# Performance work log

Hardware: AMD Instinct MI355X
Metric: run time of the kernel (lower is better)

## Reference

```python
import jax, jax.numpy as jnp
import numpy as np

B, LQ, LD, H, C = 128, 32, 512, 768, 128


def setup_inputs() -> dict:
    key = jax.random.key(0)
    ks = jax.random.split(key, 8)
    return {
        "query_hidden": jax.random.normal(ks[0], (B, LQ, H), dtype=jnp.float32),
        "doc_hidden": jax.random.normal(ks[1], (B, LD, H), dtype=jnp.float32),
        "query_mask": jax.random.randint(ks[2], (B, LQ), 0, 2, dtype=jnp.int32),
        "doc_mask": jax.random.randint(ks[3], (B, LD), 0, 2, dtype=jnp.int32),
        "W_comp": jax.random.normal(ks[4], (H, C), dtype=jnp.float32) * (1.0 / np.sqrt(H)),
        "b_comp": jax.random.normal(ks[5], (C,), dtype=jnp.float32) * 0.02,
        "w_stop": jax.random.normal(ks[6], (C, 1), dtype=jnp.float32) * (1.0 / np.sqrt(C)),
        "b_stop": jnp.ones((1,), dtype=jnp.float32),  # nn.init.constant_(bias, 1)
        "score_merger": jnp.zeros((1,), dtype=jnp.float32),
    }


def reference(query_hidden, doc_hidden, query_mask, doc_mask,
              W_comp, b_comp, w_stop, b_stop, score_merger):
    qm = query_mask.astype(bool)  # [B, LQ]
    dm = doc_mask.astype(bool)    # [B, LD]

    # encode_shared: CLS vec is the UNcompressed hidden state at position 0
    q_cls = query_hidden[:, 0, :]  # [B, H]
    d_cls = doc_hidden[:, 0, :]    # [B, H]

    # compressor (Linear H->C)
    q_vecs = jnp.einsum('blh,hc->blc', query_hidden, W_comp) + b_comp  # [B, LQ, C]
    d_tok = jnp.einsum('blh,hc->blc', doc_hidden, W_comp) + b_comp     # [B, LD, C]

    # encode_query: zero masked query tokens
    q_vecs = q_vecs * qm[..., None]

    # encode_doc: stopword reducer (relu of Linear C->1), then importance + mask
    importance = jax.nn.relu(jnp.einsum('blc,co->blo', d_tok, w_stop) + b_stop)  # [B, LD, 1]
    d_vecs = d_tok * importance * dm[..., None]

    # CLS score: dot product of (uncompressed) CLS vectors
    cls_score = jnp.sum(q_cls * d_cls, axis=-1)  # [B]

    # term score: MaxSim over doc tokens, masked sum over query tokens
    scores = jnp.einsum('bqc,bkc->bqk', q_vecs, d_vecs)      # [B, LQ, LD]
    scores = jnp.where(dm[:, None, :], scores, -1000.0)
    term = jnp.max(scores, axis=-1)                          # [B, LQ]
    term_score = jnp.sum(jnp.where(qm, term, 0.0), axis=-1)  # [B]

    w = jax.nn.sigmoid(score_merger[0])
    cls_score = cls_score * w
    term_score = term_score * (1.0 - w)
    score = cls_score + term_score
    return (score, cls_score, term_score)
```

## Files before the change

### kernel.cpp

```cpp
#include <hip/hip_runtime.h>
#include <hip/hip_bf16.h>

#define Bb 128
#define LQ 32
#define LD 512
#define Hh 768
#define Cc 128

#define DBLOCKS ((Bb * LD) / 64)

typedef short bf16x8 __attribute__((ext_vector_type(8)));
typedef short bf16x4 __attribute__((ext_vector_type(4)));
typedef float f32x4 __attribute__((ext_vector_type(4)));

__device__ __forceinline__ short f2bf(float f) {
  union { float f; unsigned u; } v;
  v.f = f;
  unsigned u = v.u + (0x7FFFu + ((v.u >> 16) & 1u));
  return (short)(u >> 16);
}

__global__ __launch_bounds__(256) void k_wt(const float* __restrict__ W,
                                            short* __restrict__ Wt) {
  int idx = blockIdx.x * 256 + threadIdx.x;
  int h = idx >> 7;
  int c = idx & 127;
  Wt[c * Hh + h] = f2bf(W[idx]);
}

__global__ __launch_bounds__(256, 3) void k_fused(
    const float* __restrict__ dh, const float* __restrict__ qh,
    const short* __restrict__ Wt, const float* __restrict__ bcomp,
    const int* __restrict__ qmask, const int* __restrict__ dmask,
    const float* __restrict__ wstop, const float* __restrict__ bstop,
    float* __restrict__ partial) {
  constexpr int ASTR = 144;
  constexpr int BSTR = 160;
  constexpr int ASZ = 64 * ASTR;
  constexpr int DSTR = 132;
  constexpr int DVB = 64 * DSTR * 4;
  __shared__ __align__(16) char smem[DVB + 32 * DSTR * 4 + 256 + 2048];

  char* bufA = smem;
  char* bufB = smem + ASZ;
  float* dvt = (float*)smem;
  float* lqt = (float*)(smem + DVB);
  int* dmsk = (int*)(smem + DVB + 32 * DSTR * 4);
  float* pm = (float*)(smem + DVB + 32 * DSTR * 4 + 256);

  const int tid = threadIdx.x;
  const int w = tid >> 6;
  const int lane = tid & 63;
  const int quad = lane >> 4;
  const int lm = lane & 15;
  const bool isq = (w < 2);

  const int b = blockIdx.x >> 3;
  const int chunk = blockIdx.x & 7;
  const long row0b = (long)b * LD + chunk * 64;

  if (tid < 64) dmsk[tid] = dmask[row0b + tid];

  const float* gA = dh + (row0b + w * 16 + (lane >> 4)) * (long)Hh + (lane & 15) * 4;
  const short* gB = Wt + (w * 32 + (lane >> 3)) * Hh + (lane & 7) * 8;
  const float* gQ = qh + ((long)b * LQ + w * 16 + lm) * Hh + quad * 8;
  const int aoff = (w * 16 + (lane >> 4)) * ASTR + (lane & 15) * 8;
  const int boff = (w * 32 + (lane >> 3)) * BSTR + (lane & 7) * 16;

  f32x4 acc[8], accq[8];
#pragma unroll
  for (int j = 0; j < 8; ++j) acc[j] = (f32x4){0.f, 0.f, 0.f, 0.f};
#pragma unroll
  for (int j = 0; j < 8; ++j) accq[j] = (f32x4){0.f, 0.f, 0.f, 0.f};

  float4 ar[4], aq[4];
  bf16x8 br[4];
#pragma unroll
  for (int i = 0; i < 4; ++i) ar[i] = *(const float4*)(gA + i * 4 * Hh);
#pragma unroll
  for (int i = 0; i < 4; ++i) br[i] = *(const bf16x8*)(gB + i * 8 * Hh);
  if (isq) {
#pragma unroll
    for (int i = 0; i < 4; ++i)
      aq[i] = *(const float4*)(gQ + (i >> 1) * 32 + (i & 1) * 4);
  }

  for (int kk = 0; kk < Hh / 64; ++kk) {
    __syncthreads();
#pragma unroll
    for (int i = 0; i < 4; ++i) {
      bf16x4 p;
      p[0] = f2bf(ar[i].x); p[1] = f2bf(ar[i].y);
      p[2] = f2bf(ar[i].z); p[3] = f2bf(ar[i].w);
      *(bf16x4*)(bufA + aoff + i * 4 * ASTR) = p;
    }
#pragma unroll
    for (int i = 0; i < 4; ++i)
      *(bf16x8*)(bufB + boff + i * 8 * BSTR) = br[i];
    __syncthreads();

    bf16x8 fq0, fq1;
    if (isq) {
      fq0[0] = f2bf(aq[0].x); fq0[1] = f2bf(aq[0].y);
      fq0[2] = f2bf(aq[0].z); fq0[3] = f2bf(aq[0].w);
      fq0[4] = f2bf(aq[1].x); fq0[5] = f2bf(aq[1].y);
      fq0[6] = f2bf(aq[1].z); fq0[7] = f2bf(aq[1].w);
      fq1[0] = f2bf(aq[2].x); fq1[1] = f2bf(aq[2].y);
      fq1[2] = f2bf(aq[2].z); fq1[3] = f2bf(aq[2].w);
      fq1[4] = f2bf(aq[3].x); fq1[5] = f2bf(aq[3].y);
      fq1[6] = f2bf(aq[3].z); fq1[7] = f2bf(aq[3].w);
    }

    {
      const long go = (kk + 1 < Hh / 64) ? (long)(kk + 1) * 64 : 0;
#pragma unroll
      for (int i = 0; i < 4; ++i) ar[i] = *(const float4*)(gA + i * 4 * Hh + go);
#pragma unroll
      for (int i = 0; i < 4; ++i) br[i] = *(const bf16x8*)(gB + i * 8 * Hh + go);
      if (isq) {
#pragma unroll
        for (int i = 0; i < 4; ++i)
          aq[i] = *(const float4*)(gQ + go + (i >> 1) * 32 + (i & 1) * 4);
      }
    }

#pragma unroll
    for (int ks = 0; ks < 2; ++ks) {
      bf16x8 fa = *(const bf16x8*)(bufA + (w * 16 + lm) * ASTR + ks * 64 + quad * 16);
      const bf16x8 fqk = (ks == 0) ? fq0 : fq1;
#pragma unroll
      for (int j = 0; j < 8; ++j) {
        bf16x8 fb = *(const bf16x8*)(bufB + (j * 16 + lm) * BSTR + ks * 64 + quad * 16);
        acc[j] = __builtin_amdgcn_mfma_f32_16x16x32_bf16(fa, fb, acc[j], 0, 0, 0);
        if (isq)
          accq[j] = __builtin_amdgcn_mfma_f32_16x16x32_bf16(fqk, fb, accq[j], 0, 0, 0);
      }
    }
  }

  __syncthreads();

  float bc[8], wsv[8];
#pragma unroll
  for (int j = 0; j < 8; ++j) bc[j] = bcomp[j * 16 + lm];
#pragma unroll
  for (int j = 0; j < 8; ++j) wsv[j] = wstop[j * 16 + lm];
  const float bs = bstop[0];

#pragma unroll
  for (int r = 0; r < 4; ++r) {
    const int lrow = w * 16 + quad * 4 + r;
    float v[8];
#pragma unroll
    for (int j = 0; j < 8; ++j) v[j] = acc[j][r] + bc[j];
    float p = 0.f;
#pragma unroll
    for (int j = 0; j < 8; ++j) p += v[j] * wsv[j];
    p += __shfl_xor(p, 1);
    p += __shfl_xor(p, 2);
    p += __shfl_xor(p, 4);
    p += __shfl_xor(p, 8);
    const float imp = fmaxf(p + bs, 0.f);
    const float scale = imp * (float)dmsk[lrow];
#pragma unroll
    for (int j = 0; j < 8; ++j) dvt[lrow * DSTR + j * 16 + lm] = v[j] * scale;
  }
  if (isq) {
    const int qrow0 = w * 16 + quad * 4;
#pragma unroll
    for (int r = 0; r < 4; ++r) {
      const int qrow = qrow0 + r;
      const float scale = (float)qmask[b * LQ + qrow];
#pragma unroll
      for (int j = 0; j < 8; ++j)
        lqt[qrow * DSTR + j * 16 + lm] = (accq[j][r] + bc[j]) * scale;
    }
  }
  __syncthreads();

  const int qt = tid & 15;
  const int kt = tid >> 4;
  const int kbase = kt * 4;
  float a[2][4];
#pragma unroll
  for (int qi = 0; qi < 2; ++qi)
#pragma unroll
    for (int ki = 0; ki < 4; ++ki) a[qi][ki] = 0.f;

  for (int c = 0; c < Cc; c += 4) {
    float4 q0 = *(float4*)&lqt[qt * DSTR + c];
    float4 q1 = *(float4*)&lqt[(qt + 16) * DSTR + c];
    float4 d0 = *(float4*)&dvt[(kbase + 0) * DSTR + c];
    float4 d1 = *(float4*)&dvt[(kbase + 1) * DSTR + c];
    float4 d2 = *(float4*)&dvt[(kbase + 2) * DSTR + c];
    float4 d3 = *(float4*)&dvt[(kbase + 3) * DSTR + c];
    a[0][0] += q0.x * d0.x + q0.y * d0.y + q0.z * d0.z + q0.w * d0.w;
    a[0][1] += q0.x * d1.x + q0.y * d1.y + q0.z * d1.z + q0.w * d1.w;
    a[0][2] += q0.x * d2.x + q0.y * d2.y + q0.z * d2.z + q0.w * d2.w;
    a[0][3] += q0.x * d3.x + q0.y * d3.y + q0.z * d3.z + q0.w * d3.w;
    a[1][0] += q1.x * d0.x + q1.y * d0.y + q1.z * d0.z + q1.w * d0.w;
    a[1][1] += q1.x * d1.x + q1.y * d1.y + q1.z * d1.z + q1.w * d1.w;
    a[1][2] += q1.x * d2.x + q1.y * d2.y + q1.z * d2.z + q1.w * d2.w;
    a[1][3] += q1.x * d3.x + q1.y * d3.y + q1.z * d3.z + q1.w * d3.w;
  }
  float m0 = -1000.f, m1 = -1000.f;
#pragma unroll
  for (int ki = 0; ki < 4; ++ki) {
    if (dmsk[kbase + ki]) {
      m0 = fmaxf(m0, a[0][ki]);
      m1 = fmaxf(m1, a[1][ki]);
    }
  }
  pm[qt * 16 + kt] = m0;
  pm[(qt + 16) * 16 + kt] = m1;
  __syncthreads();
  if (tid < LQ) {
    float mx = pm[tid * 16];
#pragma unroll
    for (int t = 1; t < 16; ++t) mx = fmaxf(mx, pm[tid * 16 + t]);
    partial[((size_t)b * LQ + tid) * 8 + chunk] = mx;
  }
}

__global__ __launch_bounds__(256) void k_final(
    const float* __restrict__ qh, const float* __restrict__ dh,
    const int* __restrict__ qmask, const float* __restrict__ partial,
    const float* __restrict__ merger, float* __restrict__ out) {
  const int b = blockIdx.x;
  const int tid = threadIdx.x;
  __shared__ float red[256];
  __shared__ float clss;
  const float* qc = qh + (size_t)b * LQ * Hh;
  const float* dc = dh + (size_t)b * LD * Hh;
  float s = 0.f;
  for (int h = tid; h < Hh; h += 256) s += qc[h] * dc[h];
  red[tid] = s;
  __syncthreads();
  for (int off = 128; off > 0; off >>= 1) {
    if (tid < off) red[tid] += red[tid + off];
    __syncthreads();
  }
  if (tid == 0) clss = red[0];
  __syncthreads();
  float t = 0.f;
  if (tid < LQ) {
    const float* pp = partial + ((size_t)b * LQ + tid) * 8;
    float mx = pp[0];
#pragma unroll
    for (int c = 1; c < 8; ++c) mx = fmaxf(mx, pp[c]);
    if (qmask[b * LQ + tid]) t = mx;
  }
  red[tid] = t;
  __syncthreads();
  for (int off = 128; off > 0; off >>= 1) {
    if (tid < off) red[tid] += red[tid + off];
    __syncthreads();
  }
  if (tid == 0) {
    float w = 1.f / (1.f + expf(-merger[0]));
    float cs = clss * w;
    float ts = red[0] * (1.f - w);
    out[b] = cs + ts;
    out[Bb + b] = cs;
    out[2 * Bb + b] = ts;
  }
}

extern "C" void kernel_launch(void* const* d_in, const int* in_sizes, int n_in,
                              void* d_out, int out_size, void* d_ws, size_t ws_size,
                              hipStream_t stream) {
  const float* qh  = (const float*)d_in[0];
  const float* dh  = (const float*)d_in[1];
  const int*   qm  = (const int*)d_in[2];
  const int*   dm  = (const int*)d_in[3];
  const float* W   = (const float*)d_in[4];
  const float* bc  = (const float*)d_in[5];
  const float* wst = (const float*)d_in[6];
  const float* bst = (const float*)d_in[7];
  const float* mrg = (const float*)d_in[8];
  float* out = (float*)d_out;

  char* ws = (char*)d_ws;
  short* Wt  = (short*)ws;
  float* prt = (float*)(ws + 196608);

  k_wt<<<(Hh * Cc) / 256, 256, 0, stream>>>(W, Wt);
  k_fused<<<DBLOCKS, 256, 0, stream>>>(dh, qh, Wt, bc, qm, dm, wst, bst, prt);
  k_final<<<Bb, 256, 0, stream>>>(qh, dh, qm, prt, mrg, out);
}
```

Measured before the change: 319.5 us.

## Load MFMA operands directly from global memory, dropping LDS staging and barriers

The GEMM main loop no longer stages the doc-hidden A tile and the transposed weight B tile through shared memory. Each lane now loads its MFMA fragments straight from global memory, converting A to bf16 in registers, and the two per-iteration __syncthreads are gone. This removes LDS write/read traffic and barrier stalls. In exchange every wave refetches the full W tile from global/L2 instead of sharing it, the B loads are not prefetched ahead, and A loads become strided per lane, which costs coalescing.

```diff
diff --git a/kernel.cpp b/kernel.cpp
--- a/kernel.cpp
+++ b/kernel.cpp
@@ -10,7 +10,6 @@
 #define DBLOCKS ((Bb * LD) / 64)
 
 typedef short bf16x8 __attribute__((ext_vector_type(8)));
-typedef short bf16x4 __attribute__((ext_vector_type(4)));
 typedef float f32x4 __attribute__((ext_vector_type(4)));
 
 __device__ __forceinline__ short f2bf(float f) {
@@ -34,19 +33,11 @@
     const int* __restrict__ qmask, const int* __restrict__ dmask,
     const float* __restrict__ wstop, const float* __restrict__ bstop,
     float* __restrict__ partial) {
-  constexpr int ASTR = 144;
-  constexpr int BSTR = 160;
-  constexpr int ASZ = 64 * ASTR;
   constexpr int DSTR = 132;
-  constexpr int DVB = 64 * DSTR * 4;
-  __shared__ __align__(16) char smem[DVB + 32 * DSTR * 4 + 256 + 2048];
-
-  char* bufA = smem;
-  char* bufB = smem + ASZ;
-  float* dvt = (float*)smem;
-  float* lqt = (float*)(smem + DVB);
-  int* dmsk = (int*)(smem + DVB + 32 * DSTR * 4);
-  float* pm = (float*)(smem + DVB + 32 * DSTR * 4 + 256);
+  __shared__ __align__(16) float dvt[64 * DSTR];
+  __shared__ __align__(16) float lqt[32 * DSTR];
+  __shared__ int dmsk[64];
+  __shared__ float pm[LQ * 16];
 
   const int tid = threadIdx.x;
   const int w = tid >> 6;
@@ -61,11 +52,9 @@
 
   if (tid < 64) dmsk[tid] = dmask[row0b + tid];
 
-  const float* gA = dh + (row0b + w * 16 + (lane >> 4)) * (long)Hh + (lane & 15) * 4;
-  const short* gB = Wt + (w * 32 + (lane >> 3)) * Hh + (lane & 7) * 8;
-  const float* gQ = qh + ((long)b * LQ + w * 16 + lm) * Hh + quad * 8;
-  const int aoff = (w * 16 + (lane >> 4)) * ASTR + (lane & 15) * 8;
-  const int boff = (w * 32 + (lane >> 3)) * BSTR + (lane & 7) * 16;
+  const float* gA = dh + (row0b + w * 16 + lm) * (long)Hh + quad * 8;
+  const float* gQ = qh + ((long)b * LQ + w * 16 + lm) * (long)Hh + quad * 8;
+  const short* gB = Wt + lm * Hh + quad * 8;
 
   f32x4 acc[8], accq[8];
 #pragma unroll
@@ -74,11 +63,9 @@
   for (int j = 0; j < 8; ++j) accq[j] = (f32x4){0.f, 0.f, 0.f, 0.f};
 
   float4 ar[4], aq[4];
-  bf16x8 br[4];
-#pragma unroll
-  for (int i = 0; i < 4; ++i) ar[i] = *(const float4*)(gA + i * 4 * Hh);
-#pragma unroll
-  for (int i = 0; i < 4; ++i) br[i] = *(const bf16x8*)(gB + i * 8 * Hh);
+#pragma unroll
+  for (int i = 0; i < 4; ++i)
+    ar[i] = *(const float4*)(gA + (i >> 1) * 32 + (i & 1) * 4);
   if (isq) {
 #pragma unroll
     for (int i = 0; i < 4; ++i)
@@ -86,20 +73,15 @@
   }
 
   for (int kk = 0; kk < Hh / 64; ++kk) {
-    __syncthreads();
-#pragma unroll
-    for (int i = 0; i < 4; ++i) {
-      bf16x4 p;
-      p[0] = f2bf(ar[i].x); p[1] = f2bf(ar[i].y);
-      p[2] = f2bf(ar[i].z); p[3] = f2bf(ar[i].w);
-      *(bf16x4*)(bufA + aoff + i * 4 * ASTR) = p;
-    }
-#pragma unroll
-    for (int i = 0; i < 4; ++i)
-      *(bf16x8*)(bufB + boff + i * 8 * BSTR) = br[i];
-    __syncthreads();
-
-    bf16x8 fq0, fq1;
+    bf16x8 fa0, fa1, fq0, fq1;
+    fa0[0] = f2bf(ar[0].x); fa0[1] = f2bf(ar[0].y);
+    fa0[2] = f2bf(ar[0].z); fa0[3] = f2bf(ar[0].w);
+    fa0[4] = f2bf(ar[1].x); fa0[5] = f2bf(ar[1].y);
+    fa0[6] = f2bf(ar[1].z); fa0[7] = f2bf(ar[1].w);
+    fa1[0] = f2bf(ar[2].x); fa1[1] = f2bf(ar[2].y);
+    fa1[2] = f2bf(ar[2].z); fa1[3] = f2bf(ar[2].w);
+    fa1[4] = f2bf(ar[3].x); fa1[5] = f2bf(ar[3].y);
+    fa1[6] = f2bf(ar[3].z); fa1[7] = f2bf(ar[3].w);
     if (isq) {
       fq0[0] = f2bf(aq[0].x); fq0[1] = f2bf(aq[0].y);
       fq0[2] = f2bf(aq[0].z); fq0[3] = f2bf(aq[0].w);
@@ -114,9 +96,8 @@
     {
       const long go = (kk + 1 < Hh / 64) ? (long)(kk + 1) * 64 : 0;
 #pragma unroll
-      for (int i = 0; i < 4; ++i) ar[i] = *(const float4*)(gA + i * 4 * Hh + go);
-#pragma unroll
-      for (int i = 0; i < 4; ++i) br[i] = *(const bf16x8*)(gB + i * 8 * Hh + go);
+      for (int i = 0; i < 4; ++i)
+        ar[i] = *(const float4*)(gA + go + (i >> 1) * 32 + (i & 1) * 4);
       if (isq) {
 #pragma unroll
         for (int i = 0; i < 4; ++i)
@@ -126,14 +107,18 @@
 
 #pragma unroll
     for (int ks = 0; ks < 2; ++ks) {
-      bf16x8 fa = *(const bf16x8*)(bufA + (w * 16 + lm) * ASTR + ks * 64 + quad * 16);
-      const bf16x8 fqk = (ks == 0) ? fq0 : fq1;
+      const bf16x8 fa = ks ? fa1 : fa0;
+      const bf16x8 fq = ks ? fq1 : fq0;
+      const long ko = (long)kk * 64 + ks * 32;
+      bf16x8 fbv[8];
+#pragma unroll
+      for (int j = 0; j < 8; ++j)
+        fbv[j] = *(const bf16x8*)(gB + j * 16 * Hh + ko);
 #pragma unroll
       for (int j = 0; j < 8; ++j) {
-        bf16x8 fb = *(const bf16x8*)(bufB + (j * 16 + lm) * BSTR + ks * 64 + quad * 16);
-        acc[j] = __builtin_amdgcn_mfma_f32_16x16x32_bf16(fa, fb, acc[j], 0, 0, 0);
+        acc[j] = __builtin_amdgcn_mfma_f32_16x16x32_bf16(fa, fbv[j], acc[j], 0, 0, 0);
         if (isq)
-          accq[j] = __builtin_amdgcn_mfma_f32_16x16x32_bf16(fqk, fb, accq[j], 0, 0, 0);
+          accq[j] = __builtin_amdgcn_mfma_f32_16x16x32_bf16(fq, fbv[j], accq[j], 0, 0, 0);
       }
     }
   }
```

Result: slower. 392.5 us (+22.9%).
